# Performance work log

Measured on AMD Instinct MI355X. Metric: run time of the kernel, lower is better.

Reference implementation:

```python
import jax, jax.numpy as jnp
import numpy as np

N = 1048576      # total reads
G = 32768        # sites (groups)
M = 32           # reads per site
DIM_COV = 16
EMB = 2
P = 8
H = 150


def setup_inputs() -> dict:
    key = jax.random.key(0)
    ks = jax.random.split(key, 12)
    x = jax.random.normal(ks[0], (N, DIM_COV), dtype=jnp.float32)
    kmer = jax.random.randint(ks[1], (N,), 0, 18, dtype=jnp.int32)
    indices = jnp.arange(N, dtype=jnp.int32).reshape(G, M)
    s = 0.05
    emb = jax.random.normal(ks[2], (18, EMB), dtype=jnp.float32) * s
    W1 = jax.random.normal(ks[3], (DIM_COV + EMB, H), dtype=jnp.float32) * s
    b1 = jnp.zeros((H,), dtype=jnp.float32)
    W2 = jax.random.normal(ks[4], (H, P), dtype=jnp.float32) * s
    b2 = jnp.zeros((P,), dtype=jnp.float32)
    W3 = jax.random.normal(ks[5], (5 * P, H), dtype=jnp.float32) * s
    b3 = jnp.zeros((H,), dtype=jnp.float32)
    W4 = jax.random.normal(ks[6], (H, 1), dtype=jnp.float32) * s
    b4 = jnp.zeros((1,), dtype=jnp.float32)
    return {"x": x, "kmer": kmer, "indices": indices, "emb": emb,
            "W1": W1, "b1": b1, "W2": W2, "b2": b2,
            "W3": W3, "b3": b3, "W4": W4, "b4": b4}


def _aggregate(h, indices):
    # h: [N, P]; indices: [G, M] -> [G, 5, P]
    g = h[indices]                               # [G, M, P]
    mean = jnp.mean(g, axis=1)
    var = jnp.var(g, axis=1, ddof=1)             # torch.var default: unbiased
    mx = jnp.max(g, axis=1)
    mn = jnp.min(g, axis=1)
    med = jnp.sort(g, axis=1)[:, (M - 1) // 2]   # torch.median: lower median
    return jnp.stack([mean, var, mn, med, mx], axis=1)


def reference(x, kmer, indices, emb, W1, b1, W2, b2, W3, b3, W4, b4):
    h = jnp.concatenate([x, emb[kmer]], axis=1)          # [N, DIM_COV+EMB]
    h = jax.nn.relu(h @ W1 + b1)                          # [N, 150]
    h = jax.nn.relu(h @ W2 + b2)                          # [N, P]
    agg = _aggregate(h, indices).reshape(-1, 5 * P)       # [G, 5P]
    z = jax.nn.relu(agg @ W3 + b3)                        # [G, 150]
    return jax.nn.sigmoid(z @ W4 + b4)                    # [G, 1]
```

## Files before the change

### kernel.cpp

```cpp
#include <hip/hip_runtime.h>
#include <hip/hip_bf16.h>
#include <hip/hip_fp16.h>
#include <math.h>

#define HDIM 150

typedef __fp16   f16x8  __attribute__((ext_vector_type(8)));
typedef __fp16   f16x2  __attribute__((ext_vector_type(2)));
typedef float    f32x4  __attribute__((ext_vector_type(4)));

__device__ __forceinline__ unsigned int pk16(float a, float b) {
    f16x2 p = __builtin_amdgcn_cvt_pkrtz(a, b);
    unsigned int w; __builtin_memcpy(&w, &p, 4);
    return w;
}

__device__ __forceinline__ f16x2 swap_halves(f16x2 v) {
    unsigned int u; __builtin_memcpy(&u, &v, 4);
    u = __builtin_amdgcn_alignbit(u, u, 16);
    f16x2 r; __builtin_memcpy(&r, &u, 4);
    return r;
}

template <typename T>
__device__ __forceinline__ void cswapT(T& a, T& b) {
    T lo = __builtin_elementwise_min(a, b);
    T hi = __builtin_elementwise_max(a, b);
    a = lo; b = hi;
}

template <typename T>
__device__ __forceinline__ void sort16t(T v[16]) {
#pragma unroll
    for (int pp = 1; pp < 16; pp <<= 1) {
#pragma unroll
        for (int k = pp; k >= 1; k >>= 1) {
#pragma unroll
            for (int j = k & (pp - 1); j + k < 16; j += 2 * k) {
#pragma unroll
                for (int i = 0; i < k; ++i) {
                    if ((i + j) / (2 * pp) == (i + j + k) / (2 * pp))
                        cswapT(v[i + j], v[i + j + k]);
                }
            }
        }
    }
}

#define FB_OFF     20480
#define AGG_OFF    20480
#define B3_OFF     26112
#define W4_OFF     26752
#define PART_OFF   27392
#define SMEM_TOTAL 35840

__global__ __launch_bounds__(256, 4) void k_all(
    const float* __restrict__ x, const int* __restrict__ kmer,
    const int* __restrict__ indices, const float* __restrict__ emb,
    const float* __restrict__ W1, const float* __restrict__ b1,
    const float* __restrict__ W2, const float* __restrict__ b2,
    const float* __restrict__ W3, const float* __restrict__ b3,
    const float* __restrict__ W4, const float* __restrict__ b4,
    float* __restrict__ out, int Gtot)
{
    __shared__ __align__(16) char smem[SMEM_TOTAL];

    const int tid  = threadIdx.x;
    const int lane = tid & 63;
    const int wv   = tid >> 6;
    const int m    = lane & 15;
    const int q    = lane >> 4;

    const int gblk  = blockIdx.x * 32;
    const int rbase = gblk * 32;

    int          rg[4];
    unsigned int egp[4];
    {
        const int lim = Gtot * 32 - 1;
#pragma unroll
        for (int g = 0; g < 4; ++g) {
            int fl = rbase + wv * 256 + g * 64 + lane;
            rg[g] = indices[fl > lim ? lim : fl];
        }
        int kk[4];
#pragma unroll
        for (int g = 0; g < 4; ++g) kk[g] = kmer[rg[g]];
        const float2* emb2 = (const float2*)emb;
#pragma unroll
        for (int g = 0; g < 4; ++g) {
            float2 e = emb2[kk[g]];
            egp[g] = pk16(e.x, e.y);
        }
    }

    uint4* fb4w = (uint4*)(smem + FB_OFF);
    {
        const int c  = tid >> 6;
        const int tn = (c < 3) ? 4 : 3;
        for (int tt = 0; tt < tn; ++tt) {
            const int tile = c * 4 + tt;
            unsigned int w[4];
#pragma unroll
            for (int dw = 0; dw < 4; ++dw) {
                const int d = tile * 4 + dw;
                float v0 = 0.f, v1 = 0.f;
                if (d < 40) {
                    int n = d >> 2, j0 = (d & 3) * 2;
                    int hid = 32 * (n >> 1) + 8 * (m >> 2) + 4 * (n & 1) + (m & 3);
                    if (hid < HDIM) {
                        int k0 = q * 8 + j0, k1 = k0 + 1;
                        v0 = (k0 < 18) ? W1[k0 * HDIM + hid] : (k0 == 18 ? b1[hid] : 0.f);
                        v1 = (k1 < 18) ? W1[k1 * HDIM + hid] : (k1 == 18 ? b1[hid] : 0.f);
                    }
                } else {
                    int kt = (d - 40) >> 2, j0 = ((d - 40) & 3) * 2;
                    int k0 = kt * 32 + q * 8 + j0, k1 = k0 + 1;
                    if (m < 8) {
                        v0 = (k0 < HDIM) ? W2[k0 * 8 + m]
                                         : (k0 == HDIM ? b2[m] : 0.f);
                        v1 = (k1 < HDIM) ? W2[k1 * 8 + m]
                                         : (k1 == HDIM ? b2[m] : 0.f);
                    }
                }
                w[dw] = pk16(v0, v1);
            }
            fb4w[tile * 64 + lane] = make_uint4(w[0], w[1], w[2], w[3]);
        }
    }
    __syncthreads();

    uint4 B16[15];
    const uint4* fb4 = (const uint4*)fb4w;
#pragma unroll
    for (int i = 0; i < 15; ++i) B16[i] = fb4[i * 64 + lane];
    const f16x8* frv = (const f16x8*)B16;
    __syncthreads();

    const char* xg = (const char*)x;

    f32x4 xa[2][2];
    auto issueTile = [&](int t) {
        int rr = __shfl(rg[t >> 2], ((t & 3) << 4) + m);
        if (q < 2) {
            const f32x4* src = (const f32x4*)(xg + (size_t)rr * 64 + (size_t)q * 32);
            xa[t & 1][0] = src[0];
            xa[t & 1][1] = src[1];
        }
    };
    issueTile(0);
    issueTile(1);

    __fp16* sH = (__fp16*)smem;
    const f32x4 zero = {0.f, 0.f, 0.f, 0.f};
    const f16x2 z2 = {};

#pragma unroll
    for (int t = 0; t < 16; ++t) {
        unsigned int ew = __shfl((int)egp[t >> 2], ((t & 3) << 4) + m);

        f16x8 bin;
#pragma unroll
        for (int j = 0; j < 8; ++j) bin[j] = (__fp16)0.f;
        if (q < 2) {
            f32x4 u0 = xa[t & 1][0];
            f32x4 u1 = xa[t & 1][1];
            f16x2 p0 = __builtin_amdgcn_cvt_pkrtz(u0[0], u0[1]);
            f16x2 p1 = __builtin_amdgcn_cvt_pkrtz(u0[2], u0[3]);
            f16x2 p2 = __builtin_amdgcn_cvt_pkrtz(u1[0], u1[1]);
            f16x2 p3 = __builtin_amdgcn_cvt_pkrtz(u1[2], u1[3]);
            bin[0] = p0[0]; bin[1] = p0[1]; bin[2] = p1[0]; bin[3] = p1[1];
            bin[4] = p2[0]; bin[5] = p2[1]; bin[6] = p3[0]; bin[7] = p3[1];
        } else if (q == 2) {
            f16x2 ep; __builtin_memcpy(&ep, &ew, 4);
            bin[0] = ep[0]; bin[1] = ep[1];
            bin[2] = (__fp16)1.0f;
        }

        if (t < 14) issueTile(t + 2);

        f32x4 c2a = zero, c2b = zero;
#pragma unroll
        for (int kt = 0; kt < 5; ++kt) {
            f32x4 ca = __builtin_amdgcn_mfma_f32_16x16x32_f16(frv[2 * kt],     bin, zero, 0, 0, 0);
            f32x4 cb = __builtin_amdgcn_mfma_f32_16x16x32_f16(frv[2 * kt + 1], bin, zero, 0, 0, 0);
            f16x2 h01 = __builtin_elementwise_max(__builtin_amdgcn_cvt_pkrtz(ca[0], ca[1]), z2);
            f16x2 h23 = __builtin_elementwise_max(__builtin_amdgcn_cvt_pkrtz(ca[2], ca[3]), z2);
            f16x2 h45 = __builtin_elementwise_max(__builtin_amdgcn_cvt_pkrtz(cb[0], cb[1]), z2);
            f16x2 h67 = __builtin_elementwise_max(__builtin_amdgcn_cvt_pkrtz(cb[2], cb[3]), z2);
            f16x8 bh;
            bh[0] = h01[0]; bh[1] = h01[1]; bh[2] = h23[0]; bh[3] = h23[1];
            bh[4] = h45[0]; bh[5] = h45[1]; bh[6] = h67[0]; bh[7] = h67[1];
            if (kt == 4 && q == 2) bh[6] = (__fp16)1.0f;
            if (kt & 1) c2b = __builtin_amdgcn_mfma_f32_16x16x32_f16(frv[10 + kt], bh, c2b, 0, 0, 0);
            else        c2a = __builtin_amdgcn_mfma_f32_16x16x32_f16(frv[10 + kt], bh, c2a, 0, 0, 0);
        }

        if (q < 2) {
            int br   = wv * 256 + t * 16 + m;
            int site = br >> 5, mm = br & 31;
            float s0 = c2a[0] + c2b[0], s1 = c2a[1] + c2b[1];
            float s2 = c2a[2] + c2b[2], s3 = c2a[3] + c2b[3];
            f16x2 o01 = __builtin_elementwise_max(__builtin_amdgcn_cvt_pkrtz(s0, s1), z2);
            f16x2 o23 = __builtin_elementwise_max(__builtin_amdgcn_cvt_pkrtz(s2, s3), z2);
            __fp16* hb = sH + site * 320 + mm;
            hb[(q * 4 + 0) * 40] = o01[0];
            hb[(q * 4 + 1) * 40] = o01[1];
            hb[(q * 4 + 2) * 40] = o23[0];
            hb[(q * 4 + 3) * 40] = o23[1];
        }
    }

    float* sAgg = (float*)(smem + AGG_OFF);
    float* sPart= (float*)(smem + PART_OFF);

    const int fl_ = tid >> 2, fdw = tid & 3;
    const int fm = fl_ & 15, fq = fl_ >> 4;
    unsigned int hw[20];
#pragma unroll
    for (int j = 0; j < 20; ++j) {
        int jt = j >> 1, kc = j & 1;
        int row = jt * 16 + fm;
        int k0  = kc * 32 + fq * 8 + fdw * 2;
        float v0 = (k0     < 40 && row < HDIM) ? W3[k0 * HDIM + row]       : 0.f;
        float v1 = (k0 + 1 < 40 && row < HDIM) ? W3[(k0 + 1) * HDIM + row] : 0.f;
        hw[j] = pk16(v0, v1);
    }
    float b3r = 0.f, w4r = 0.f;
    if (tid < 160) {
        b3r = (tid < HDIM) ? b3[tid] : 0.f;
        w4r = (tid < HDIM) ? W4[tid] : 0.f;
    }

    const int sg = tid >> 3, p = tid & 7;
    {
        const __fp16* hp = sH + sg * 320 + p * 40;
        uint4 rr4[4];
#pragma unroll
        for (int c = 0; c < 4; ++c) rr4[c] = *(const uint4*)(hp + c * 8);
        f16x2 v[16];
        __builtin_memcpy(v, rr4, 64);

        float sum = 0.f, sumsq = 0.f;
        const f16x2 ones = {(__fp16)1.0f, (__fp16)1.0f};
#pragma unroll
        for (int k = 0; k < 16; ++k) {
            sum   = __builtin_amdgcn_fdot2(v[k], ones, sum, false);
            sumsq = __builtin_amdgcn_fdot2(v[k], v[k], sumsq, false);
        }

        sort16t(v);

        float mn = fminf((float)v[0][0],  (float)v[0][1]);
        float mx = fmaxf((float)v[15][0], (float)v[15][1]);

        f16x2 medv = __builtin_elementwise_min(v[0], swap_halves(v[15]));
#pragma unroll
        for (int i = 1; i < 16; ++i)
            medv = __builtin_elementwise_max(
                medv, __builtin_elementwise_min(v[i], swap_halves(v[15 - i])));
        float med = (float)medv[0];

        float mean = sum * (1.f / 32.f);
        float var  = fmaxf((sumsq - 32.f * mean * mean) * (1.f / 31.f), 0.f);
        sAgg[sg * 44 + 0 * 8 + p] = mean;
        sAgg[sg * 44 + 1 * 8 + p] = var;
        sAgg[sg * 44 + 2 * 8 + p] = mn;
        sAgg[sg * 44 + 3 * 8 + p] = med;
        sAgg[sg * 44 + 4 * 8 + p] = mx;
    }
    __syncthreads();

    unsigned int* hfT = (unsigned int*)smem;
#pragma unroll
    for (int j = 0; j < 20; ++j)
        hfT[j * 256 + tid] = hw[j];
    float* sB3 = (float*)(smem + B3_OFF);
    float* sW4 = (float*)(smem + W4_OFF);
    if (tid < 160) { sB3[tid] = b3r; sW4[tid] = w4r; }
    __syncthreads();

    const int jthalf = wv >> 1, sh = wv & 1;
    uint4 HF[10];
    {
        const uint4* hfv = (const uint4*)hfT;
#pragma unroll
        for (int i = 0; i < 10; ++i) {
            int jt = jthalf * 5 + (i >> 1), kc = i & 1;
            HF[i] = hfv[(jt * 2 + kc) * 64 + lane];
        }
    }
    const f16x8* hf = (const f16x8*)HF;

    const int site = sh * 16 + m;
    const float* ar = sAgg + site * 44;
    f16x8 bh0, bl0, bh1, bl1;
    {
        float4 a0 = *(const float4*)(ar + q * 8);
        float4 a1 = *(const float4*)(ar + q * 8 + 4);
        float va[8] = {a0.x, a0.y, a0.z, a0.w, a1.x, a1.y, a1.z, a1.w};
#pragma unroll
        for (int j = 0; j < 8; ++j) {
            __fp16 hi = (__fp16)va[j];
            bh0[j] = hi;
            bl0[j] = (__fp16)(va[j] - (float)hi);
        }
    }
    if (q == 0) {
        float4 a0 = *(const float4*)(ar + 32);
        float4 a1 = *(const float4*)(ar + 36);
        float va[8] = {a0.x, a0.y, a0.z, a0.w, a1.x, a1.y, a1.z, a1.w};
#pragma unroll
        for (int j = 0; j < 8; ++j) {
            __fp16 hi = (__fp16)va[j];
            bh1[j] = hi;
            bl1[j] = (__fp16)(va[j] - (float)hi);
        }
    } else {
#pragma unroll
        for (int j = 0; j < 8; ++j) { bh1[j] = (__fp16)0.f; bl1[j] = (__fp16)0.f; }
    }

    const float4* b3v = (const float4*)sB3;
    const float4* w4v = (const float4*)sW4;
    float sacc = 0.f;
#pragma unroll
    for (int jj = 0; jj < 5; ++jj) {
        int jt = jthalf * 5 + jj;
        float4 bi = b3v[jt * 4 + q];
        f32x4 acc = {bi.x, bi.y, bi.z, bi.w};
        acc = __builtin_amdgcn_mfma_f32_16x16x32_f16(hf[jj * 2 + 0], bh0, acc, 0, 0, 0);
        acc = __builtin_amdgcn_mfma_f32_16x16x32_f16(hf[jj * 2 + 0], bl0, acc, 0, 0, 0);
        acc = __builtin_amdgcn_mfma_f32_16x16x32_f16(hf[jj * 2 + 1], bh1, acc, 0, 0, 0);
        acc = __builtin_amdgcn_mfma_f32_16x16x32_f16(hf[jj * 2 + 1], bl1, acc, 0, 0, 0);
        float4 w4q = w4v[jt * 4 + q];
        sacc = fmaf(fmaxf(acc[0], 0.f), w4q.x, sacc);
        sacc = fmaf(fmaxf(acc[1], 0.f), w4q.y, sacc);
        sacc = fmaf(fmaxf(acc[2], 0.f), w4q.z, sacc);
        sacc = fmaf(fmaxf(acc[3], 0.f), w4q.w, sacc);
    }
    sacc += __shfl_xor(sacc, 16);
    sacc += __shfl_xor(sacc, 32);
    if (jthalf == 1 && lane < 16) sPart[sh * 16 + lane] = sacc;
    __syncthreads();
    if (jthalf == 0 && lane < 16) {
        int s2 = sh * 16 + lane;
        float zf = sacc + sPart[s2] + b4[0];
        if (gblk + s2 < Gtot) out[gblk + s2] = 1.f / (1.f + expf(-zf));
    }
}

extern "C" void kernel_launch(void* const* d_in, const int* in_sizes, int n_in,
                              void* d_out, int out_size, void* d_ws, size_t ws_size,
                              hipStream_t stream) {
    const float* x       = (const float*)d_in[0];
    const int*   kmer    = (const int*)  d_in[1];
    const int*   indices = (const int*)  d_in[2];
    const float* emb     = (const float*)d_in[3];
    const float* W1      = (const float*)d_in[4];
    const float* b1      = (const float*)d_in[5];
    const float* W2      = (const float*)d_in[6];
    const float* b2      = (const float*)d_in[7];
    const float* W3      = (const float*)d_in[8];
    const float* b3      = (const float*)d_in[9];
    const float* W4      = (const float*)d_in[10];
    const float* b4      = (const float*)d_in[11];

    float* out = (float*)d_out;
    const int G = out_size;

    const int grid = (G + 31) / 32;
    k_all<<<grid, 256, 0, stream>>>(x, kmer, indices, emb,
                                    W1, b1, W2, b2, W3, b3, W4, b4,
                                    out, G);
}
```

Measured before the change: 31.30 us.

## Hoist x prefetch before weight staging and pack paired f16 H stores into dwords

Moves the first two x-tile global loads ahead of the kmer/embedding gathers and the weight staging, so their latency overlaps the setup work. Alternates tiles so each even tile's layer-2 outputs are held in registers and combined with the odd tile's into packed f16x2 words. This replaces four 16-bit LDS stores per tile with four 32-bit stores every two tiles. The in-site element order changes to pair read m with read m+16, which relies on the later aggregation being order-independent.

```diff
diff --git a/kernel.cpp b/kernel.cpp
--- a/kernel.cpp
+++ b/kernel.cpp
@@ -74,8 +74,7 @@
     const int gblk  = blockIdx.x * 32;
     const int rbase = gblk * 32;
 
-    int          rg[4];
-    unsigned int egp[4];
+    int rg[4];
     {
         const int lim = Gtot * 32 - 1;
 #pragma unroll
@@ -83,6 +82,24 @@
             int fl = rbase + wv * 256 + g * 64 + lane;
             rg[g] = indices[fl > lim ? lim : fl];
         }
+    }
+
+    const char* xg = (const char*)x;
+
+    f32x4 xa[2][2];
+    auto issueTile = [&](int t) {
+        int rr = __shfl(rg[t >> 2], ((t & 3) << 4) + m);
+        if (q < 2) {
+            const f32x4* src = (const f32x4*)(xg + (size_t)rr * 64 + (size_t)q * 32);
+            xa[t & 1][0] = src[0];
+            xa[t & 1][1] = src[1];
+        }
+    };
+    issueTile(0);
+    issueTile(1);
+
+    unsigned int egp[4];
+    {
         int kk[4];
 #pragma unroll
         for (int g = 0; g < 4; ++g) kk[g] = kmer[rg[g]];
@@ -137,23 +154,11 @@
     const f16x8* frv = (const f16x8*)B16;
     __syncthreads();
 
-    const char* xg = (const char*)x;
-
-    f32x4 xa[2][2];
-    auto issueTile = [&](int t) {
-        int rr = __shfl(rg[t >> 2], ((t & 3) << 4) + m);
-        if (q < 2) {
-            const f32x4* src = (const f32x4*)(xg + (size_t)rr * 64 + (size_t)q * 32);
-            xa[t & 1][0] = src[0];
-            xa[t & 1][1] = src[1];
-        }
-    };
-    issueTile(0);
-    issueTile(1);
-
-    __fp16* sH = (__fp16*)smem;
+    unsigned int* sH32 = (unsigned int*)smem;
     const f32x4 zero = {0.f, 0.f, 0.f, 0.f};
     const f16x2 z2 = {};
+
+    float se0 = 0.f, se1 = 0.f, se2 = 0.f, se3 = 0.f;
 
 #pragma unroll
     for (int t = 0; t < 16; ++t) {
@@ -197,17 +202,27 @@
         }
 
         if (q < 2) {
-            int br   = wv * 256 + t * 16 + m;
-            int site = br >> 5, mm = br & 31;
             float s0 = c2a[0] + c2b[0], s1 = c2a[1] + c2b[1];
             float s2 = c2a[2] + c2b[2], s3 = c2a[3] + c2b[3];
-            f16x2 o01 = __builtin_elementwise_max(__builtin_amdgcn_cvt_pkrtz(s0, s1), z2);
-            f16x2 o23 = __builtin_elementwise_max(__builtin_amdgcn_cvt_pkrtz(s2, s3), z2);
-            __fp16* hb = sH + site * 320 + mm;
-            hb[(q * 4 + 0) * 40] = o01[0];
-            hb[(q * 4 + 1) * 40] = o01[1];
-            hb[(q * 4 + 2) * 40] = o23[0];
-            hb[(q * 4 + 3) * 40] = o23[1];
+            if (!(t & 1)) {
+                se0 = s0; se1 = s1; se2 = s2; se3 = s3;
+            } else {
+                int site = wv * 8 + (t >> 1);
+                f16x2 w0 = __builtin_elementwise_max(__builtin_amdgcn_cvt_pkrtz(se0, s0), z2);
+                f16x2 w1 = __builtin_elementwise_max(__builtin_amdgcn_cvt_pkrtz(se1, s1), z2);
+                f16x2 w2 = __builtin_elementwise_max(__builtin_amdgcn_cvt_pkrtz(se2, s2), z2);
+                f16x2 w3 = __builtin_elementwise_max(__builtin_amdgcn_cvt_pkrtz(se3, s3), z2);
+                unsigned int u0, u1, u2, u3;
+                __builtin_memcpy(&u0, &w0, 4);
+                __builtin_memcpy(&u1, &w1, 4);
+                __builtin_memcpy(&u2, &w2, 4);
+                __builtin_memcpy(&u3, &w3, 4);
+                unsigned int* hb = sH32 + site * 160 + m;
+                hb[(q * 4 + 0) * 20] = u0;
+                hb[(q * 4 + 1) * 20] = u1;
+                hb[(q * 4 + 2) * 20] = u2;
+                hb[(q * 4 + 3) * 20] = u3;
+            }
         }
     }
 
@@ -234,10 +249,10 @@
 
     const int sg = tid >> 3, p = tid & 7;
     {
-        const __fp16* hp = sH + sg * 320 + p * 40;
+        const uint4* hp4 = (const uint4*)(sH32 + sg * 160 + p * 20);
         uint4 rr4[4];
 #pragma unroll
-        for (int c = 0; c < 4; ++c) rr4[c] = *(const uint4*)(hp + c * 8);
+        for (int c = 0; c < 4; ++c) rr4[c] = hp4[c];
         f16x2 v[16];
         __builtin_memcpy(v, rr4, 64);
 
```

Result: slower. 32.20 us (+2.8%).
